# Performance work log

Measured on AMD Instinct MI355X. Metric: run time of the kernel, lower is better.

The kernel has to match this reference:

```python
import jax, jax.numpy as jnp
import numpy as np

LUT_DIM = 33
CTX_DIM = 128


def _identity_lut(dim):
    coords = jnp.linspace(0.0, 1.0, dim)
    r, g, b = jnp.meshgrid(coords, coords, coords, indexing='ij')
    return jnp.stack([r, g, b], axis=-1)  # [dim, dim, dim, 3], axes (r,g,b)


def setup_inputs() -> dict:
    key = jax.random.key(0)
    ks = jax.random.split(key, 8)
    B, H, W = 4, 512, 512
    image = jax.random.normal(ks[0], (B, 3, H, W), dtype=jnp.float32)
    spatial_context = jax.random.normal(ks[1], (B, CTX_DIM, H, W), dtype=jnp.float32)
    s = 0.05
    params = {
        'base_lut': _identity_lut(LUT_DIM),
        'W1': jax.random.normal(ks[2], (128, CTX_DIM), dtype=jnp.float32) * s,
        'b1': jnp.zeros((128,), dtype=jnp.float32),
        'W2': jax.random.normal(ks[3], (64, 128), dtype=jnp.float32) * s,
        'b2': jnp.zeros((64,), dtype=jnp.float32),
        'W3': jax.random.normal(ks[4], (3, 64), dtype=jnp.float32) * s,
        'b3': jnp.zeros((3,), dtype=jnp.float32),
        'offset_scale': jnp.float32(0.1),
    }
    return {'image': image, 'spatial_context': spatial_context, **params}


def _conv1x1(x, W, b):
    # x: [B,Cin,H,W], W: [Cout,Cin]
    return jnp.einsum('bchw,oc->bohw', x, W) + b[None, :, None, None]


def _trilinear_lut(lut_flat, gx, gy, gz, dim):
    # lut_flat: [3, dim^3] (flattened over z,y,x = r,g,b axes)
    # gx,gy,gz: [B,H,W] float coords in [0, dim-1]; border padding via clamp
    fmax = jnp.float32(dim - 1)
    gx = jnp.clip(gx, 0.0, fmax)
    gy = jnp.clip(gy, 0.0, fmax)
    gz = jnp.clip(gz, 0.0, fmax)
    x0 = jnp.floor(gx).astype(jnp.int32)
    y0 = jnp.floor(gy).astype(jnp.int32)
    z0 = jnp.floor(gz).astype(jnp.int32)
    x1 = jnp.minimum(x0 + 1, dim - 1)
    y1 = jnp.minimum(y0 + 1, dim - 1)
    z1 = jnp.minimum(z0 + 1, dim - 1)
    fx = gx - x0.astype(gx.dtype)
    fy = gy - y0.astype(gy.dtype)
    fz = gz - z0.astype(gz.dtype)

    def gather(zi, yi, xi):
        idx = (zi * dim + yi) * dim + xi  # [B,H,W]
        return lut_flat[:, idx]  # [3,B,H,W]

    c000 = gather(z0, y0, x0); c001 = gather(z0, y0, x1)
    c010 = gather(z0, y1, x0); c011 = gather(z0, y1, x1)
    c100 = gather(z1, y0, x0); c101 = gather(z1, y0, x1)
    c110 = gather(z1, y1, x0); c111 = gather(z1, y1, x1)

    fx = fx[None]; fy = fy[None]; fz = fz[None]
    c00 = c000 * (1 - fx) + c001 * fx
    c01 = c010 * (1 - fx) + c011 * fx
    c10 = c100 * (1 - fx) + c101 * fx
    c11 = c110 * (1 - fx) + c111 * fx
    c0 = c00 * (1 - fy) + c01 * fy
    c1 = c10 * (1 - fy) + c11 * fy
    out = c0 * (1 - fz) + c1 * fz  # [3,B,H,W]
    return jnp.transpose(out, (1, 0, 2, 3))  # [B,3,H,W]


def reference(image, spatial_context, base_lut, W1, b1, W2, b2, W3, b3, offset_scale):
    dim = base_lut.shape[0]
    gelu = lambda v: jax.nn.gelu(v, approximate=False)
    h = gelu(_conv1x1(spatial_context, W1, b1))
    h = gelu(_conv1x1(h, W2, b2))
    offset = jnp.tanh(_conv1x1(h, W3, b3)) * offset_scale  # [B,3,H,W]

    img01 = jnp.clip((image + 1.0) * 0.5, 0.0, 1.0)
    # grid_sample convention: grid channel0 (R)->x->last LUT axis (b),
    # channel1 (G)->y->g axis, channel2 (B)->z->r axis; align_corners=True.
    scale = jnp.float32(dim - 1)
    gx = img01[:, 0] * scale  # R -> b axis
    gy = img01[:, 1] * scale  # G -> g axis
    gz = img01[:, 2] * scale  # B -> r axis
    # base_lut [r,g,b,3] -> channels-first [3, r(=z), g(=y), b(=x)] -> flatten
    lut_flat = jnp.transpose(base_lut, (3, 0, 1, 2)).reshape(3, dim * dim * dim)
    sampled = _trilinear_lut(lut_flat, gx, gy, gz, dim)  # [B,3,H,W]
    return sampled * 2.0 - 1.0 + offset
```

## Files before the change

kernel.cpp:

```cpp
#include <hip/hip_runtime.h>
#include <stdint.h>

#define HW 262144
#define LDIM 33

typedef __bf16 bf16x8 __attribute__((ext_vector_type(8)));
typedef __bf16 bf16x2 __attribute__((ext_vector_type(2)));
typedef float  f32x4  __attribute__((ext_vector_type(4)));

union BF8 { bf16x8 v; unsigned u[4]; };

__device__ __forceinline__ unsigned pk2(float a, float b) {
  bf16x2 p; p[0] = (__bf16)a; p[1] = (__bf16)b;
  return __builtin_bit_cast(unsigned, p);
}
__device__ __forceinline__ float exp2_hw(float x) {
  return __builtin_amdgcn_exp2f(x);
}
__device__ __forceinline__ float tanh_fast(float x) {
  float t = exp2_hw(x * 2.8853900818f);
  return 1.0f - __fdividef(2.0f, t + 1.0f);
}
__device__ __forceinline__ float gelu_t(float x) {
  float x2 = x * x;
  float p2 = x * fmaf(0.1029425216f, x2, 2.3021667f);
  float r  = __fdividef(1.0f, exp2_hw(p2) + 1.0f);
  return fmaf(-x, r, x);
}

__global__ __launch_bounds__(512, 4) void local3dlut_kernel(
    const float* __restrict__ img,  const float* __restrict__ ctx,
    const float* __restrict__ lut,  const float* __restrict__ W1,
    const float* __restrict__ b1,   const float* __restrict__ W2,
    const float* __restrict__ b2,   const float* __restrict__ W3,
    const float* __restrict__ b3,   const float* __restrict__ oscp,
    float* __restrict__ out)
{
  __shared__ uint4 smem4[4096];
  char* sm = (char*)smem4;
  const int t    = threadIdx.x;
  const int lane = t & 63;
  const int wv   = t >> 6;
  const int n    = lane & 15;
  const int q    = lane >> 4;

  #pragma unroll
  for (int rep = 0; rep < 8; ++rep) {
    int f4 = t + 512 * rep;
    float4 v = ((const float4*)W1)[f4];
    int fi = f4 << 2;
    int o = fi >> 7, k = fi & 127;
    char* dst = sm + o * 256 + (((k >> 3) ^ (o & 15)) << 4) + ((k & 7) << 1);
    *(uint2*)dst = make_uint2(pk2(v.x, v.y), pk2(v.z, v.w));
  }
  #pragma unroll
  for (int rep = 0; rep < 4; ++rep) {
    int f4 = t + 512 * rep;
    float4 v = ((const float4*)W2)[f4];
    int fi = f4 << 2;
    int o = fi >> 7, k = fi & 127;
    char* dst = sm + 32768 + o * 256 + (((k >> 3) ^ (o & 15)) << 4) + ((k & 7) << 1);
    *(uint2*)dst = make_uint2(pk2(v.x, v.y), pk2(v.z, v.w));
  }
  __syncthreads();

  float b1r[8];
  #pragma unroll
  for (int i = 0; i < 8; ++i) b1r[i] = b1[i * 16 + n];
  float b2r[4];
  #pragma unroll
  for (int i = 0; i < 4; ++i) b2r[i] = b2[i * 16 + n];
  BF8 w3a[2];
  #pragma unroll
  for (int ks3 = 0; ks3 < 2; ++ks3) {
    #pragma unroll
    for (int m = 0; m < 4; ++m) {
      float e0 = 0.f, e1 = 0.f;
      if (n < 3) {
        e0 = W3[n * 64 + ks3 * 32 + q * 8 + 2 * m];
        e1 = W3[n * 64 + ks3 * 32 + q * 8 + 2 * m + 1];
      }
      w3a[ks3].u[m] = pk2(e0, e1);
    }
  }
  const float b3a0 = b3[0], b3a1 = b3[1], b3a2 = b3[2];
  const float osc  = oscp[0];

  const int p0   = blockIdx.x * 1024;
  const int bi   = p0 >> 18;
  const int sblk = p0 & (HW - 1);
  const float* ctxB = ctx + (size_t)bi * ((size_t)128 * HW);
  const float* imgB = img + (size_t)bi * ((size_t)3 * HW);
  float*       outB = out + (size_t)bi * ((size_t)3 * HW);
  char* hb = sm + 49152 + wv * 2048;

  #pragma unroll 1
  for (int it = 0; it < 8; ++it) {
    const int sw = sblk + it * 128 + wv * 16;

    const int spf = sw + n;
    const float rr = imgB[spf];
    const float gg = imgB[HW + spf];
    const float bb = imgB[2 * HW + spf];

    BF8 a1[4];
    {
      const int sA = sw + n;
      #pragma unroll
      for (int ks = 0; ks < 4; ++ks) {
        const float* cb = ctxB + (size_t)(ks * 32 + q * 8) * HW + sA;
        float v0 = cb[0];
        float v1 = cb[(size_t)1 * HW];
        float v2 = cb[(size_t)2 * HW];
        float v3 = cb[(size_t)3 * HW];
        float v4 = cb[(size_t)4 * HW];
        float v5 = cb[(size_t)5 * HW];
        float v6 = cb[(size_t)6 * HW];
        float v7 = cb[(size_t)7 * HW];
        a1[ks].u[0] = pk2(v0, v1);
        a1[ks].u[1] = pk2(v2, v3);
        a1[ks].u[2] = pk2(v4, v5);
        a1[ks].u[3] = pk2(v6, v7);
      }
    }

    float fx, fy, fz;
    float c000, c001, c010, c011, c100, c101, c110, c111;
    {
      float gx = fminf(fmaxf(fmaf(rr, 16.f, 16.f), 0.f), 32.f);
      float gy = fminf(fmaxf(fmaf(gg, 16.f, 16.f), 0.f), 32.f);
      float gz = fminf(fmaxf(fmaf(bb, 16.f, 16.f), 0.f), 32.f);
      int x0 = (int)gx, y0 = (int)gy, z0 = (int)gz;
      fx = gx - (float)x0; fy = gy - (float)y0; fz = gz - (float)z0;
      int x1 = min(x0 + 1, 32), y1 = min(y0 + 1, 32), z1 = min(z0 + 1, 32);
      int zy00 = (z0 * LDIM + y0) * LDIM, zy01 = (z0 * LDIM + y1) * LDIM;
      int zy10 = (z1 * LDIM + y0) * LDIM, zy11 = (z1 * LDIM + y1) * LDIM;
      const int chq = (q < 3) ? q : 2;
      const float* L = lut;
      c000 = L[(zy00 + x0) * 3 + chq]; c001 = L[(zy00 + x1) * 3 + chq];
      c010 = L[(zy01 + x0) * 3 + chq]; c011 = L[(zy01 + x1) * 3 + chq];
      c100 = L[(zy10 + x0) * 3 + chq]; c101 = L[(zy10 + x1) * 3 + chq];
      c110 = L[(zy11 + x0) * 3 + chq]; c111 = L[(zy11 + x1) * 3 + chq];
    }

    f32x4 acc2[4];
    #pragma unroll
    for (int j = 0; j < 4; ++j) { f32x4 z = {0.f,0.f,0.f,0.f}; acc2[j] = z; }

    #pragma unroll
    for (int half = 0; half < 2; ++half) {
      f32x4 acc1[4];
      #pragma unroll
      for (int j = 0; j < 4; ++j) { f32x4 z = {0.f,0.f,0.f,0.f}; acc1[j] = z; }

      #pragma unroll
      for (int ks = 0; ks < 4; ++ks) {
        #pragma unroll
        for (int nt4 = 0; nt4 < 4; ++nt4) {
          int row = (half * 4 + nt4) * 16 + n;
          bf16x8 bw = *(const bf16x8*)(sm + row * 256 + ((((ks << 2) + q) ^ n) << 4));
          acc1[nt4] = __builtin_amdgcn_mfma_f32_16x16x32_bf16(a1[ks].v, bw, acc1[nt4], 0, 0, 0);
        }
      }
      #pragma unroll
      for (int nt4 = 0; nt4 < 4; ++nt4) {
        int fl = nt4 * 16 + n;
        int kgf = fl >> 3;
        #pragma unroll
        for (int r = 0; r < 4; ++r) {
          int px = (q << 2) + r;
          float hv = gelu_t(acc1[nt4][r] + b1r[half * 4 + nt4]);
          *(__bf16*)(hb + px * 128 + ((kgf ^ (px & 7)) << 4) + ((fl & 7) << 1)) = (__bf16)hv;
        }
      }
      #pragma unroll
      for (int ks2 = 0; ks2 < 2; ++ks2) {
        bf16x8 a2 = *(const bf16x8*)(hb + n * 128 + ((((ks2 << 2) + q) ^ (n & 7)) << 4));
        #pragma unroll
        for (int nt2 = 0; nt2 < 4; ++nt2) {
          int row = nt2 * 16 + n;
          int kg2 = half * 8 + (ks2 << 2) + q;
          bf16x8 bw = *(const bf16x8*)(sm + 32768 + row * 256 + ((kg2 ^ n) << 4));
          acc2[nt2] = __builtin_amdgcn_mfma_f32_16x16x32_bf16(a2, bw, acc2[nt2], 0, 0, 0);
        }
      }
    }

    #pragma unroll
    for (int nt2 = 0; nt2 < 4; ++nt2) {
      int kgW = (nt2 << 1) + (n >> 3);
      #pragma unroll
      for (int r = 0; r < 4; ++r) {
        int px = (q << 2) + r;
        float hv = gelu_t(acc2[nt2][r] + b2r[nt2]);
        *(__bf16*)(hb + px * 128 + ((kgW ^ (px & 7)) << 4) + ((n & 7) << 1)) = (__bf16)hv;
      }
    }

    f32x4 acc3 = {0.f, 0.f, 0.f, 0.f};
    #pragma unroll
    for (int ks3 = 0; ks3 < 2; ++ks3) {
      bf16x8 hf = *(const bf16x8*)(hb + n * 128 + ((((ks3 << 2) + q) ^ (n & 7)) << 4));
      acc3 = __builtin_amdgcn_mfma_f32_16x16x32_bf16(w3a[ks3].v, hf, acc3, 0, 0, 0);
    }
    const int ba = n << 2;
    float d0 = __int_as_float(__builtin_amdgcn_ds_bpermute(ba, __float_as_int(acc3[0])));
    float d1 = __int_as_float(__builtin_amdgcn_ds_bpermute(ba, __float_as_int(acc3[1])));
    float d2 = __int_as_float(__builtin_amdgcn_ds_bpermute(ba, __float_as_int(acc3[2])));

    if (q < 3) {
      float sel  = (q == 0) ? d0   : ((q == 1) ? d1   : d2);
      float bsel = (q == 0) ? b3a0 : ((q == 1) ? b3a1 : b3a2);
      float ov = tanh_fast(sel + bsel) * osc;

      float c00 = c000 + fx * (c001 - c000);
      float c01 = c010 + fx * (c011 - c010);
      float c10 = c100 + fx * (c101 - c100);
      float c11 = c110 + fx * (c111 - c110);
      float ca  = c00 + fy * (c01 - c00);
      float cb2 = c10 + fy * (c11 - c10);
      float so  = ca + fz * (cb2 - ca);
      outB[q * HW + sw + n] = so * 2.f - 1.f + ov;
    }
  }
}

extern "C" void kernel_launch(void* const* d_in, const int* in_sizes, int n_in,
                              void* d_out, int out_size, void* d_ws, size_t ws_size,
                              hipStream_t stream) {
  const float* img = (const float*)d_in[0];
  const float* ctx = (const float*)d_in[1];
  const float* lut = (const float*)d_in[2];
  const float* W1  = (const float*)d_in[3];
  const float* b1  = (const float*)d_in[4];
  const float* W2  = (const float*)d_in[5];
  const float* b2  = (const float*)d_in[6];
  const float* W3  = (const float*)d_in[7];
  const float* b3  = (const float*)d_in[8];
  const float* osc = (const float*)d_in[9];
  float* out = (float*)d_out;
  local3dlut_kernel<<<dim3(1024), dim3(512), 0, stream>>>(
      img, ctx, lut, W1, b1, W2, b2, W3, b3, osc, out);
}
```

Measured before the change: 789.3 us.

## Split LUT trilinear sampling out of MLP kernel into separate pass

Splits the fused kernel in two. The MLP kernel now writes only the tanh offset to the output, and a second lightweight kernel reads the image and that offset, does trilinear LUT sampling with all three channels per thread, and writes the final result. This removes the image loads, the LUT gathers and their register pressure from the MFMA-heavy kernel, at the cost of an extra launch and an extra read and write pass over the output.

```diff
diff --git a/kernel.cpp b/kernel.cpp
--- a/kernel.cpp
+++ b/kernel.cpp
@@ -28,9 +28,14 @@
   return fmaf(-x, r, x);
 }
 
-__global__ __launch_bounds__(512, 4) void local3dlut_kernel(
-    const float* __restrict__ img,  const float* __restrict__ ctx,
-    const float* __restrict__ lut,  const float* __restrict__ W1,
+struct F3 { float x, y, z; };
+__device__ __forceinline__ F3 lerp3(F3 a, F3 b, float f) {
+  F3 r; r.x = a.x + f * (b.x - a.x); r.y = a.y + f * (b.y - a.y);
+  r.z = a.z + f * (b.z - a.z); return r;
+}
+
+__global__ __launch_bounds__(512, 4) void mlp_offset_kernel(
+    const float* __restrict__ ctx,  const float* __restrict__ W1,
     const float* __restrict__ b1,   const float* __restrict__ W2,
     const float* __restrict__ b2,   const float* __restrict__ W3,
     const float* __restrict__ b3,   const float* __restrict__ oscp,
@@ -90,18 +95,12 @@
   const int bi   = p0 >> 18;
   const int sblk = p0 & (HW - 1);
   const float* ctxB = ctx + (size_t)bi * ((size_t)128 * HW);
-  const float* imgB = img + (size_t)bi * ((size_t)3 * HW);
   float*       outB = out + (size_t)bi * ((size_t)3 * HW);
   char* hb = sm + 49152 + wv * 2048;
 
   #pragma unroll 1
   for (int it = 0; it < 8; ++it) {
     const int sw = sblk + it * 128 + wv * 16;
-
-    const int spf = sw + n;
-    const float rr = imgB[spf];
-    const float gg = imgB[HW + spf];
-    const float bb = imgB[2 * HW + spf];
 
     BF8 a1[4];
     {
@@ -124,25 +123,6 @@
       }
     }
 
-    float fx, fy, fz;
-    float c000, c001, c010, c011, c100, c101, c110, c111;
-    {
-      float gx = fminf(fmaxf(fmaf(rr, 16.f, 16.f), 0.f), 32.f);
-      float gy = fminf(fmaxf(fmaf(gg, 16.f, 16.f), 0.f), 32.f);
-      float gz = fminf(fmaxf(fmaf(bb, 16.f, 16.f), 0.f), 32.f);
-      int x0 = (int)gx, y0 = (int)gy, z0 = (int)gz;
-      fx = gx - (float)x0; fy = gy - (float)y0; fz = gz - (float)z0;
-      int x1 = min(x0 + 1, 32), y1 = min(y0 + 1, 32), z1 = min(z0 + 1, 32);
-      int zy00 = (z0 * LDIM + y0) * LDIM, zy01 = (z0 * LDIM + y1) * LDIM;
-      int zy10 = (z1 * LDIM + y0) * LDIM, zy11 = (z1 * LDIM + y1) * LDIM;
-      const int chq = (q < 3) ? q : 2;
-      const float* L = lut;
-      c000 = L[(zy00 + x0) * 3 + chq]; c001 = L[(zy00 + x1) * 3 + chq];
-      c010 = L[(zy01 + x0) * 3 + chq]; c011 = L[(zy01 + x1) * 3 + chq];
-      c100 = L[(zy10 + x0) * 3 + chq]; c101 = L[(zy10 + x1) * 3 + chq];
-      c110 = L[(zy11 + x0) * 3 + chq]; c111 = L[(zy11 + x1) * 3 + chq];
-    }
-
     f32x4 acc2[4];
     #pragma unroll
     for (int j = 0; j < 4; ++j) { f32x4 z = {0.f,0.f,0.f,0.f}; acc2[j] = z; }
@@ -211,18 +191,48 @@
     if (q < 3) {
       float sel  = (q == 0) ? d0   : ((q == 1) ? d1   : d2);
       float bsel = (q == 0) ? b3a0 : ((q == 1) ? b3a1 : b3a2);
-      float ov = tanh_fast(sel + bsel) * osc;
-
-      float c00 = c000 + fx * (c001 - c000);
-      float c01 = c010 + fx * (c011 - c010);
-      float c10 = c100 + fx * (c101 - c100);
-      float c11 = c110 + fx * (c111 - c110);
-      float ca  = c00 + fy * (c01 - c00);
-      float cb2 = c10 + fy * (c11 - c10);
-      float so  = ca + fz * (cb2 - ca);
-      outB[q * HW + sw + n] = so * 2.f - 1.f + ov;
-    }
-  }
+      outB[q * HW + sw + n] = tanh_fast(sel + bsel) * osc;
+    }
+  }
+}
+
+__global__ __launch_bounds__(256) void lut_apply_kernel(
+    const float* __restrict__ img, const float* __restrict__ lut,
+    float* __restrict__ out)
+{
+  const int p  = blockIdx.x * 256 + threadIdx.x;
+  const int b  = p >> 18;
+  const int sp = p & (HW - 1);
+  const float* imgB = img + (size_t)b * ((size_t)3 * HW);
+  float*       outB = out + (size_t)b * ((size_t)3 * HW);
+
+  const float rr = imgB[sp];
+  const float gg = imgB[HW + sp];
+  const float bb = imgB[2 * HW + sp];
+  const float o0 = outB[sp];
+  const float o1 = outB[HW + sp];
+  const float o2 = outB[2 * HW + sp];
+
+  float gx = fminf(fmaxf(fmaf(rr, 16.f, 16.f), 0.f), 32.f);
+  float gy = fminf(fmaxf(fmaf(gg, 16.f, 16.f), 0.f), 32.f);
+  float gz = fminf(fmaxf(fmaf(bb, 16.f, 16.f), 0.f), 32.f);
+  int x0 = (int)gx, y0 = (int)gy, z0 = (int)gz;
+  float fx = gx - (float)x0, fy = gy - (float)y0, fz = gz - (float)z0;
+  int x1 = min(x0 + 1, 32), y1 = min(y0 + 1, 32), z1 = min(z0 + 1, 32);
+  int zy00 = (z0 * LDIM + y0) * LDIM, zy01 = (z0 * LDIM + y1) * LDIM;
+  int zy10 = (z1 * LDIM + y0) * LDIM, zy11 = (z1 * LDIM + y1) * LDIM;
+  const F3* L3 = (const F3*)lut;
+  F3 c000 = L3[zy00 + x0], c001 = L3[zy00 + x1];
+  F3 c010 = L3[zy01 + x0], c011 = L3[zy01 + x1];
+  F3 c100 = L3[zy10 + x0], c101 = L3[zy10 + x1];
+  F3 c110 = L3[zy11 + x0], c111 = L3[zy11 + x1];
+  F3 c00 = lerp3(c000, c001, fx), c01 = lerp3(c010, c011, fx);
+  F3 c10 = lerp3(c100, c101, fx), c11 = lerp3(c110, c111, fx);
+  F3 ca  = lerp3(c00, c01, fy),   cb2 = lerp3(c10, c11, fy);
+  F3 so  = lerp3(ca, cb2, fz);
+  outB[sp]          = fmaf(so.x, 2.f, -1.f) + o0;
+  outB[HW + sp]     = fmaf(so.y, 2.f, -1.f) + o1;
+  outB[2 * HW + sp] = fmaf(so.z, 2.f, -1.f) + o2;
 }
 
 extern "C" void kernel_launch(void* const* d_in, const int* in_sizes, int n_in,
@@ -239,6 +249,7 @@
   const float* b3  = (const float*)d_in[8];
   const float* osc = (const float*)d_in[9];
   float* out = (float*)d_out;
-  local3dlut_kernel<<<dim3(1024), dim3(512), 0, stream>>>(
-      img, ctx, lut, W1, b1, W2, b2, W3, b3, osc, out);
-}
+  mlp_offset_kernel<<<dim3(1024), dim3(512), 0, stream>>>(
+      ctx, W1, b1, W2, b2, W3, b3, osc, out);
+  lut_apply_kernel<<<dim3(4096), dim3(256), 0, stream>>>(img, lut, out);
+}
```

After: 794.6 us. No clear change (+0.7%).

## Swap MFMA operand order to get transposed hidden tiles and packed LDS writes

Applied to the files above, without the earlier changes.

The layer-1 and layer-2 MFMAs now take their operands in swapped order, so each lane's accumulator holds four consecutive hidden features for one pixel. GELU outputs can then be packed into one 8-byte LDS store per tile instead of four scalar bf16 stores. Biases are preloaded per lane to match the new accumulator layout. The block shrinks to 256 threads with 2048 blocks and 56KB of LDS, which changes occupancy and the number of times the weights are staged per block.

```diff
diff --git a/kernel.cpp b/kernel.cpp
--- a/kernel.cpp
+++ b/kernel.cpp
@@ -28,7 +28,7 @@
   return fmaf(-x, r, x);
 }
 
-__global__ __launch_bounds__(512, 4) void local3dlut_kernel(
+__global__ __launch_bounds__(256, 2) void local3dlut_kernel(
     const float* __restrict__ img,  const float* __restrict__ ctx,
     const float* __restrict__ lut,  const float* __restrict__ W1,
     const float* __restrict__ b1,   const float* __restrict__ W2,
@@ -36,7 +36,7 @@
     const float* __restrict__ b3,   const float* __restrict__ oscp,
     float* __restrict__ out)
 {
-  __shared__ uint4 smem4[4096];
+  __shared__ uint4 smem4[3584];
   char* sm = (char*)smem4;
   const int t    = threadIdx.x;
   const int lane = t & 63;
@@ -45,8 +45,8 @@
   const int q    = lane >> 4;
 
   #pragma unroll
-  for (int rep = 0; rep < 8; ++rep) {
-    int f4 = t + 512 * rep;
+  for (int rep = 0; rep < 16; ++rep) {
+    int f4 = t + 256 * rep;
     float4 v = ((const float4*)W1)[f4];
     int fi = f4 << 2;
     int o = fi >> 7, k = fi & 127;
@@ -54,8 +54,8 @@
     *(uint2*)dst = make_uint2(pk2(v.x, v.y), pk2(v.z, v.w));
   }
   #pragma unroll
-  for (int rep = 0; rep < 4; ++rep) {
-    int f4 = t + 512 * rep;
+  for (int rep = 0; rep < 8; ++rep) {
+    int f4 = t + 256 * rep;
     float4 v = ((const float4*)W2)[f4];
     int fi = f4 << 2;
     int o = fi >> 7, k = fi & 127;
@@ -64,12 +64,16 @@
   }
   __syncthreads();
 
-  float b1r[8];
-  #pragma unroll
-  for (int i = 0; i < 8; ++i) b1r[i] = b1[i * 16 + n];
-  float b2r[4];
-  #pragma unroll
-  for (int i = 0; i < 4; ++i) b2r[i] = b2[i * 16 + n];
+  float b1l[8][4];
+  #pragma unroll
+  for (int i = 0; i < 8; ++i)
+    #pragma unroll
+    for (int r = 0; r < 4; ++r) b1l[i][r] = b1[i * 16 + (q << 2) + r];
+  float b2l[4][4];
+  #pragma unroll
+  for (int i = 0; i < 4; ++i)
+    #pragma unroll
+    for (int r = 0; r < 4; ++r) b2l[i][r] = b2[i * 16 + (q << 2) + r];
   BF8 w3a[2];
   #pragma unroll
   for (int ks3 = 0; ks3 < 2; ++ks3) {
@@ -86,17 +90,20 @@
   const float b3a0 = b3[0], b3a1 = b3[1], b3a2 = b3[2];
   const float osc  = oscp[0];
 
-  const int p0   = blockIdx.x * 1024;
+  const int p0   = blockIdx.x * 512;
   const int bi   = p0 >> 18;
   const int sblk = p0 & (HW - 1);
   const float* ctxB = ctx + (size_t)bi * ((size_t)128 * HW);
   const float* imgB = img + (size_t)bi * ((size_t)3 * HW);
   float*       outB = out + (size_t)bi * ((size_t)3 * HW);
   char* hb = sm + 49152 + wv * 2048;
+  char* hrow = hb + n * 128;
+  const int nsw = n & 7;
+  const int woff = (q & 1) << 3;
 
   #pragma unroll 1
   for (int it = 0; it < 8; ++it) {
-    const int sw = sblk + it * 128 + wv * 16;
+    const int sw = sblk + it * 64 + wv * 16;
 
     const int spf = sw + n;
     const float rr = imgB[spf];
@@ -159,48 +166,47 @@
         for (int nt4 = 0; nt4 < 4; ++nt4) {
           int row = (half * 4 + nt4) * 16 + n;
           bf16x8 bw = *(const bf16x8*)(sm + row * 256 + ((((ks << 2) + q) ^ n) << 4));
-          acc1[nt4] = __builtin_amdgcn_mfma_f32_16x16x32_bf16(a1[ks].v, bw, acc1[nt4], 0, 0, 0);
+          acc1[nt4] = __builtin_amdgcn_mfma_f32_16x16x32_bf16(bw, a1[ks].v, acc1[nt4], 0, 0, 0);
         }
       }
       #pragma unroll
       for (int nt4 = 0; nt4 < 4; ++nt4) {
-        int fl = nt4 * 16 + n;
-        int kgf = fl >> 3;
-        #pragma unroll
-        for (int r = 0; r < 4; ++r) {
-          int px = (q << 2) + r;
-          float hv = gelu_t(acc1[nt4][r] + b1r[half * 4 + nt4]);
-          *(__bf16*)(hb + px * 128 + ((kgf ^ (px & 7)) << 4) + ((fl & 7) << 1)) = (__bf16)hv;
-        }
+        float g0 = gelu_t(acc1[nt4][0] + b1l[half * 4 + nt4][0]);
+        float g1 = gelu_t(acc1[nt4][1] + b1l[half * 4 + nt4][1]);
+        float g2 = gelu_t(acc1[nt4][2] + b1l[half * 4 + nt4][2]);
+        float g3 = gelu_t(acc1[nt4][3] + b1l[half * 4 + nt4][3]);
+        int kg = (nt4 << 1) + (q >> 1);
+        char* dst = hrow + ((kg ^ nsw) << 4) + woff;
+        *(uint2*)dst = make_uint2(pk2(g0, g1), pk2(g2, g3));
       }
       #pragma unroll
       for (int ks2 = 0; ks2 < 2; ++ks2) {
-        bf16x8 a2 = *(const bf16x8*)(hb + n * 128 + ((((ks2 << 2) + q) ^ (n & 7)) << 4));
+        bf16x8 a2 = *(const bf16x8*)(hrow + ((((ks2 << 2) + q) ^ nsw) << 4));
         #pragma unroll
         for (int nt2 = 0; nt2 < 4; ++nt2) {
           int row = nt2 * 16 + n;
           int kg2 = half * 8 + (ks2 << 2) + q;
           bf16x8 bw = *(const bf16x8*)(sm + 32768 + row * 256 + ((kg2 ^ n) << 4));
-          acc2[nt2] = __builtin_amdgcn_mfma_f32_16x16x32_bf16(a2, bw, acc2[nt2], 0, 0, 0);
+          acc2[nt2] = __builtin_amdgcn_mfma_f32_16x16x32_bf16(bw, a2, acc2[nt2], 0, 0, 0);
         }
       }
     }
 
     #pragma unroll
     for (int nt2 = 0; nt2 < 4; ++nt2) {
-      int kgW = (nt2 << 1) + (n >> 3);
-      #pragma unroll
-      for (int r = 0; r < 4; ++r) {
-        int px = (q << 2) + r;
-        float hv = gelu_t(acc2[nt2][r] + b2r[nt2]);
-        *(__bf16*)(hb + px * 128 + ((kgW ^ (px & 7)) << 4) + ((n & 7) << 1)) = (__bf16)hv;
-      }
+      float g0 = gelu_t(acc2[nt2][0] + b2l[nt2][0]);
+      float g1 = gelu_t(acc2[nt2][1] + b2l[nt2][1]);
+      float g2 = gelu_t(acc2[nt2][2] + b2l[nt2][2]);
+      float g3 = gelu_t(acc2[nt2][3] + b2l[nt2][3]);
+      int kg = (nt2 << 1) + (q >> 1);
+      char* dst = hrow + ((kg ^ nsw) << 4) + woff;
+      *(uint2*)dst = make_uint2(pk2(g0, g1), pk2(g2, g3));
     }
 
     f32x4 acc3 = {0.f, 0.f, 0.f, 0.f};
     #pragma unroll
     for (int ks3 = 0; ks3 < 2; ++ks3) {
-      bf16x8 hf = *(const bf16x8*)(hb + n * 128 + ((((ks3 << 2) + q) ^ (n & 7)) << 4));
+      bf16x8 hf = *(const bf16x8*)(hrow + ((((ks3 << 2) + q) ^ nsw) << 4));
       acc3 = __builtin_amdgcn_mfma_f32_16x16x32_bf16(w3a[ks3].v, hf, acc3, 0, 0, 0);
     }
     const int ba = n << 2;
@@ -239,6 +245,6 @@
   const float* b3  = (const float*)d_in[8];
   const float* osc = (const float*)d_in[9];
   float* out = (float*)d_out;
-  local3dlut_kernel<<<dim3(1024), dim3(512), 0, stream>>>(
+  local3dlut_kernel<<<dim3(2048), dim3(256), 0, stream>>>(
       img, ctx, lut, W1, b1, W2, b2, W3, b3, osc, out);
 }
```

New measurement: 777.3 us. Within noise of the previous version (-1.5%).
